# Kernel tuning notes

Measured on AMD Instinct MI355X. Metric: run time of the kernel, lower is better.

The kernel has to match this reference:

```python
import jax, jax.numpy as jnp
import numpy as np

N_WIDTH = 64
N_ORDER = 4
N_ELEMENTS = 64
N_NODES = N_ELEMENTS * N_ORDER + 1  # 257
N_SAMPLES = 4096
X_MIN = 0.0
X_MAX = 1.0


def _lagrange(x, n_order):
    # x: [S, W] reference coords in [-1, 1] -> [S, W, P] basis values
    nodes = np.linspace(-1.0, 1.0, n_order + 1)
    cols = []
    for j in range(n_order + 1):
        p = jnp.ones_like(x)
        for m in range(n_order + 1):
            if m != j:
                p = p * (x - nodes[m]) / (nodes[j] - nodes[m])
        cols.append(p)
    return jnp.stack(cols, axis=-1)


def _dlagrange(x, n_order):
    nodes = np.linspace(-1.0, 1.0, n_order + 1)
    cols = []
    for j in range(n_order + 1):
        y = jnp.zeros_like(x)
        for i in range(n_order + 1):
            if i != j:
                k = jnp.full_like(x, 1.0 / (nodes[j] - nodes[i]))
                for m in range(n_order + 1):
                    if m != i and m != j:
                        k = k * (x - nodes[m]) / (nodes[j] - nodes[m])
                y = y + k
        cols.append(y)
    return jnp.stack(cols, axis=-1)


def _ddlagrange(x, n_order):
    nodes = np.linspace(-1.0, 1.0, n_order + 1)
    cols = []
    for j in range(n_order + 1):
        y = jnp.zeros_like(x)
        for i in range(n_order + 1):
            if i != j:
                k_sum = jnp.zeros_like(x)
                for m in range(n_order + 1):
                    if m != i and m != j:
                        k_prod = jnp.full_like(x, 1.0 / (nodes[j] - nodes[m]))
                        for n in range(n_order + 1):
                            if n != i and n != j and n != m:
                                k_prod = k_prod * (x - nodes[n]) / (nodes[j] - nodes[n])
                        k_sum = k_sum + k_prod
                y = y + k_sum / (nodes[j] - nodes[i])
        cols.append(y)
    return jnp.stack(cols, axis=-1)


def setup_inputs() -> dict:
    key = jax.random.key(0)
    k1, k2 = jax.random.split(key)
    x = jax.random.uniform(k1, (N_SAMPLES,), minval=X_MIN, maxval=X_MAX, dtype=jnp.float32)
    # xavier_normal_ for [n_width, n_nodes]: std = sqrt(2 / (fan_in + fan_out))
    std = np.sqrt(2.0 / (N_WIDTH + N_NODES)).astype(np.float32)
    weight = jax.random.normal(k2, (N_WIDTH, N_NODES), dtype=jnp.float32) * std
    return {"x": x, "weight": weight}


def reference(x, weight):
    if x.ndim != 2:
        x = jnp.repeat(x[:, None], N_WIDTH, axis=-1)  # [S, W]
    S = x.shape[0]
    x_shift = (N_NODES - 1) * (x - X_MIN) / (X_MAX - X_MIN)
    id_el = jnp.clip(jnp.floor(x_shift / N_ORDER), 0, N_ELEMENTS - 1)
    nodes_in_l = (id_el * N_ORDER).astype(jnp.int32)  # [S, W]
    # to_ref with node_r - node_l == n_order
    x_t = 2.0 * (x_shift - nodes_in_l) / N_ORDER - 1.0
    delta_x = 0.5 * N_ORDER * (X_MAX - X_MIN) / (N_NODES - 1)

    phi_l = _lagrange(x_t, N_ORDER)                       # [S, W, P]
    dphi_l = _dlagrange(x_t, N_ORDER) / delta_x
    ddphi_l = _ddlagrange(x_t, N_ORDER) / (delta_x ** 2)

    P = N_ORDER + 1
    idx = nodes_in_l[:, :, None] + jnp.arange(P)          # [S, W, P] global node ids
    si = jnp.arange(S)[:, None, None]
    wi = jnp.arange(N_WIDTH)[None, :, None]

    def scatter(vals):
        return jnp.zeros((S, N_WIDTH, N_NODES), vals.dtype).at[si, wi, idx].set(vals)

    phi_ikp = scatter(phi_l)
    dphi_ikp = scatter(dphi_l)
    ddphi_ikp = scatter(ddphi_l)

    t_ik = jnp.einsum('kp,ikp->ik', weight, phi_ikp)
    dt_ik = jnp.einsum('kp,ikp->ik', weight, dphi_ikp)
    ddt_ik = jnp.einsum('kp,ikp->ik', weight, ddphi_ikp)
    return (t_ik, dt_ik, ddt_ik, phi_ikp, dphi_ikp, ddphi_ikp, jnp.float32(delta_x))
```

## Files before the change

### kernel.cpp

```cpp
#include <hip/hip_runtime.h>

#define NS     4096
#define NW     64
#define NNODES 257
#define SW     (NS * NW)
#define ROW    (NW * NNODES)
#define ROW4   (ROW / 4)
#define SWN    ((size_t)NS * NW * NNODES)

__device__ __constant__ const float P4[5] = { (float)( 2.0/3.0), (float)(-8.0/3.0),  4.0f, (float)(-8.0/3.0), (float)( 2.0/3.0) };
__device__ __constant__ const float P3[5] = { (float)(-2.0/3.0), (float)( 4.0/3.0),  0.0f, (float)(-4.0/3.0), (float)( 2.0/3.0) };
__device__ __constant__ const float P2[5] = { (float)(-1.0/6.0), (float)( 8.0/3.0), -5.0f, (float)( 8.0/3.0), (float)(-1.0/6.0) };
__device__ __constant__ const float P1[5] = { (float)( 1.0/6.0), (float)(-4.0/3.0),  0.0f, (float)( 4.0/3.0), (float)(-1.0/6.0) };
__device__ __constant__ const float P0[5] = { 0.0f, 0.0f, 1.0f, 0.0f, 0.0f };

__device__ __constant__ const float D3[5] = { (float)( 1024.0/3.0), (float)(-4096.0/3.0),  2048.0f, (float)(-4096.0/3.0), (float)(1024.0/3.0) };
__device__ __constant__ const float D2[5] = { -256.0f, 512.0f, 0.0f, -512.0f, 256.0f };
__device__ __constant__ const float D1[5] = { (float)( -128.0/3.0), (float)( 2048.0/3.0), -1280.0f, (float)( 2048.0/3.0), (float)(-128.0/3.0) };
__device__ __constant__ const float D0[5] = { (float)(   64.0/3.0), (float)( -512.0/3.0),     0.0f, (float)(  512.0/3.0), (float)( -64.0/3.0) };

__device__ __constant__ const float E2[5] = { 131072.0f, -524288.0f, 786432.0f, -524288.0f, 131072.0f };
__device__ __constant__ const float E1[5] = { -65536.0f,  131072.0f,      0.0f, -131072.0f,  65536.0f };
__device__ __constant__ const float E0[5] = { (float)(-16384.0/3.0), (float)(262144.0/3.0), -163840.0f, (float)(262144.0/3.0), (float)(-16384.0/3.0) };

__global__ __launch_bounds__(256) void kann_all(
    const float* __restrict__ x,
    const float* __restrict__ weight,
    float* __restrict__ out)
{
    const int i   = blockIdx.x;
    const int tid = threadIdx.x;

    __shared__ __align__(16) float tmpl[3][1028];

    const float xs = 256.0f * x[i];
    float fel = floorf(xs * 0.25f);
    fel = fminf(fmaxf(fel, 0.0f), 63.0f);
    const int   b = (int)fel * 4;
    const float t = 0.5f * (xs - (float)b) - 1.0f;

    float bas[3][5];
    #pragma unroll
    for (int j = 0; j < 5; ++j) {
        bas[0][j] = (((P4[j]*t + P3[j])*t + P2[j])*t + P1[j])*t + P0[j];
        bas[1][j] = ((D3[j]*t + D2[j])*t + D1[j])*t + D0[j];
        bas[2][j] = (E2[j]*t + E1[j])*t + E0[j];
    }

    if (tid < NW) {
        const float* wrow = weight + tid * NNODES + b;
        float s0 = 0.0f, s1 = 0.0f, s2 = 0.0f;
        #pragma unroll
        for (int j = 0; j < 5; ++j) {
            const float w = wrow[j];
            s0 += w * bas[0][j];
            s1 += w * bas[1][j];
            s2 += w * bas[2][j];
        }
        out[(size_t)i * NW + tid]               = s0;
        out[SW + (size_t)i * NW + tid]          = s1;
        out[2 * (size_t)SW + (size_t)i * NW + tid] = s2;
    }
    if (i == 0 && tid == 64)
        out[3 * (size_t)SW + 3 * SWN] = 0.0078125f;

    #pragma unroll
    for (int a = 0; a < 3; ++a) {
        for (int idx = tid; idx < 1028; idx += 256) {
            const int q = (idx - (idx >> 8)) >> 8;
            const int r = idx - ((q << 8) + q);
            const int d = r - b;
            float v = 0.0f;
            v = (d == 0) ? bas[a][0] : v;
            v = (d == 1) ? bas[a][1] : v;
            v = (d == 2) ? bas[a][2] : v;
            v = (d == 3) ? bas[a][3] : v;
            v = (d == 4) ? bas[a][4] : v;
            tmpl[a][idx] = v;
        }
    }
    __syncthreads();

    float* big = out + 3 * (size_t)SW + (size_t)i * ROW;
    #pragma unroll
    for (int a = 0; a < 3; ++a) {
        float4* reg = reinterpret_cast<float4*>(big + (size_t)a * SWN);
        const float4* t4 = reinterpret_cast<const float4*>(tmpl[a]);
        #pragma unroll 4
        for (int o = tid; o < ROW4; o += 256) {
            const int q  = (o - (o >> 8)) >> 8;
            const int om = o - ((q << 8) + q);
            reg[o] = t4[om];
        }
    }
}

extern "C" void kernel_launch(void* const* d_in, const int* in_sizes, int n_in,
                              void* d_out, int out_size, void* d_ws, size_t ws_size,
                              hipStream_t stream) {
    const float* x      = (const float*)d_in[0];
    const float* weight = (const float*)d_in[1];
    float* out          = (float*)d_out;
    kann_all<<<NS, 256, 0, stream>>>(x, weight, out);
}
```

Before: 164.7 us.

## Split into bulk zero-fill kernel and sparse nonzero-writing kernel

Replaces the single kernel, which built per-sample shared-memory templates and streamed full rows, with two kernels. The first is a grid-stride float4 zero fill of the three large scattered tensors. The second computes the dot products and has 192 threads each write only the aligned 16-float window holding the five nonzero basis values of its row. This removes the shared-memory staging, the barrier and the per-element index arithmetic, at the cost of a second launch and rewriting a few cache lines after the zero pass. The total write traffic stays about the same since the zero pass still covers the whole output.

```diff
diff --git a/kernel.cpp b/kernel.cpp
--- a/kernel.cpp
+++ b/kernel.cpp
@@ -7,6 +7,9 @@
 #define ROW    (NW * NNODES)
 #define ROW4   (ROW / 4)
 #define SWN    ((size_t)NS * NW * NNODES)
+#define NG4    ((size_t)3 * SWN / 4)
+
+typedef float v4f __attribute__((ext_vector_type(4)));
 
 __device__ __constant__ const float P4[5] = { (float)( 2.0/3.0), (float)(-8.0/3.0),  4.0f, (float)(-8.0/3.0), (float)( 2.0/3.0) };
 __device__ __constant__ const float P3[5] = { (float)(-2.0/3.0), (float)( 4.0/3.0),  0.0f, (float)(-4.0/3.0), (float)( 2.0/3.0) };
@@ -23,7 +26,16 @@
 __device__ __constant__ const float E1[5] = { -65536.0f,  131072.0f,      0.0f, -131072.0f,  65536.0f };
 __device__ __constant__ const float E0[5] = { (float)(-16384.0/3.0), (float)(262144.0/3.0), -163840.0f, (float)(262144.0/3.0), (float)(-16384.0/3.0) };
 
-__global__ __launch_bounds__(256) void kann_all(
+__global__ __launch_bounds__(256) void k_zero(float* __restrict__ big)
+{
+    const v4f z = { 0.0f, 0.0f, 0.0f, 0.0f };
+    v4f* p = reinterpret_cast<v4f*>(big);
+    const size_t stride = (size_t)4096 * 256;
+    for (size_t g = (size_t)blockIdx.x * 256 + threadIdx.x; g < NG4; g += stride)
+        p[g] = z;
+}
+
+__global__ __launch_bounds__(256) void k_values(
     const float* __restrict__ x,
     const float* __restrict__ weight,
     float* __restrict__ out)
@@ -31,20 +43,18 @@
     const int i   = blockIdx.x;
     const int tid = threadIdx.x;
 
-    __shared__ __align__(16) float tmpl[3][1028];
-
     const float xs = 256.0f * x[i];
     float fel = floorf(xs * 0.25f);
     fel = fminf(fmaxf(fel, 0.0f), 63.0f);
     const int   b = (int)fel * 4;
     const float t = 0.5f * (xs - (float)b) - 1.0f;
 
-    float bas[3][5];
+    float p0[5], p1[5], p2[5];
     #pragma unroll
     for (int j = 0; j < 5; ++j) {
-        bas[0][j] = (((P4[j]*t + P3[j])*t + P2[j])*t + P1[j])*t + P0[j];
-        bas[1][j] = ((D3[j]*t + D2[j])*t + D1[j])*t + D0[j];
-        bas[2][j] = (E2[j]*t + E1[j])*t + E0[j];
+        p0[j] = (((P4[j]*t + P3[j])*t + P2[j])*t + P1[j])*t + P0[j];
+        p1[j] = ((D3[j]*t + D2[j])*t + D1[j])*t + D0[j];
+        p2[j] = (E2[j]*t + E1[j])*t + E0[j];
     }
 
     if (tid < NW) {
@@ -53,44 +63,60 @@
         #pragma unroll
         for (int j = 0; j < 5; ++j) {
             const float w = wrow[j];
-            s0 += w * bas[0][j];
-            s1 += w * bas[1][j];
-            s2 += w * bas[2][j];
+            s0 += w * p0[j]; s1 += w * p1[j]; s2 += w * p2[j];
         }
-        out[(size_t)i * NW + tid]               = s0;
-        out[SW + (size_t)i * NW + tid]          = s1;
+        out[(size_t)i * NW + tid]                  = s0;
+        out[SW + (size_t)i * NW + tid]             = s1;
         out[2 * (size_t)SW + (size_t)i * NW + tid] = s2;
     }
-    if (i == 0 && tid == 64)
+    if (i == 0 && tid == 192)
         out[3 * (size_t)SW + 3 * SWN] = 0.0078125f;
 
-    #pragma unroll
-    for (int a = 0; a < 3; ++a) {
-        for (int idx = tid; idx < 1028; idx += 256) {
-            const int q = (idx - (idx >> 8)) >> 8;
-            const int r = idx - ((q << 8) + q);
-            const int d = r - b;
-            float v = 0.0f;
-            v = (d == 0) ? bas[a][0] : v;
-            v = (d == 1) ? bas[a][1] : v;
-            v = (d == 2) ? bas[a][2] : v;
-            v = (d == 3) ? bas[a][3] : v;
-            v = (d == 4) ? bas[a][4] : v;
-            tmpl[a][idx] = v;
+    if (tid < 192) {
+        const int a   = tid >> 6;
+        const int row = tid & 63;
+
+        float ba[5];
+        #pragma unroll
+        for (int j = 0; j < 5; ++j)
+            ba[j] = (a == 0) ? p0[j] : ((a == 1) ? p1[j] : p2[j]);
+
+        const int m   = row * NNODES + b;
+        const int rho = row & 3;
+
+        float w0[4], w1[4];
+        #pragma unroll
+        for (int c = 0; c < 4; ++c) {
+            float v0 = 0.0f, v1 = 0.0f;
+            #pragma unroll
+            for (int r = 0; r < 4; ++r) {
+                if (r <= c) v0 = (rho == r) ? ba[c - r]     : v0;
+                if (r >= c) v1 = (rho == r) ? ba[4 + c - r] : v1;
+            }
+            w0[c] = v0; w1[c] = v1;
         }
-    }
-    __syncthreads();
 
-    float* big = out + 3 * (size_t)SW + (size_t)i * ROW;
-    #pragma unroll
-    for (int a = 0; a < 3; ++a) {
-        float4* reg = reinterpret_cast<float4*>(big + (size_t)a * SWN);
-        const float4* t4 = reinterpret_cast<const float4*>(tmpl[a]);
-        #pragma unroll 4
-        for (int o = tid; o < ROW4; o += 256) {
-            const int q  = (o - (o >> 8)) >> 8;
-            const int om = o - ((q << 8) + q);
-            reg[o] = t4[om];
+        const int q  = (m >> 2) & 3;
+        const int O0 = (m >> 4) << 2;
+
+        v4f* r4 = reinterpret_cast<v4f*>(
+            out + 3 * (size_t)SW + (size_t)a * SWN + (size_t)i * ROW);
+
+        const v4f z  = { 0.0f, 0.0f, 0.0f, 0.0f };
+        const v4f W0 = { w0[0], w0[1], w0[2], w0[3] };
+        const v4f W1 = { w1[0], w1[1], w1[2], w1[3] };
+
+        #pragma unroll
+        for (int s = 0; s < 4; ++s) {
+            const v4f t1 = (s == q + 1) ? W1 : z;
+            const v4f vv = (s == q)     ? W0 : t1;
+            r4[O0 + s] = vv;
+        }
+        if (q == 3) {
+            r4[O0 + 4] = W1;
+            r4[O0 + 5] = z;
+            r4[O0 + 6] = z;
+            r4[O0 + 7] = z;
         }
     }
 }
@@ -101,5 +127,8 @@
     const float* x      = (const float*)d_in[0];
     const float* weight = (const float*)d_in[1];
     float* out          = (float*)d_out;
-    kann_all<<<NS, 256, 0, stream>>>(x, weight, out);
+    float* big          = out + 3 * (size_t)SW;
+
+    k_zero<<<4096, 256, 0, stream>>>(big);
+    k_values<<<NS, 256, 0, stream>>>(x, weight, out);
 }
```

Result: slower. 275.9 us (+67.5%).
